# Kernel optimization log

Hardware: AMD Instinct MI355X
Metric: run time of the kernel (lower is better)

Reference implementation:

```python
import jax, jax.numpy as jnp
import numpy as np
import math

B, S, H, NH, WIN = 2, 2048, 1024, 16, 1024
HD = H // NH


def _ln(x, g, b, eps=1e-5):
    mu = jnp.mean(x, axis=-1, keepdims=True)
    var = jnp.var(x, axis=-1, keepdims=True)
    return (x - mu) * jax.lax.rsqrt(var + eps) * g + b


def setup_inputs() -> dict:
    key = jax.random.key(0)
    ks = jax.random.split(key, 16)
    w = lambda k, shp: jax.random.normal(k, shp, dtype=jnp.float32) * 0.02
    d = {
        "hidden_states": jax.random.normal(ks[0], (B, S, H), dtype=jnp.float32),
        "window_pos_bias": jax.random.normal(ks[1], (1, NH, 2 * WIN + 1, 2 * WIN + 1), dtype=jnp.float32) * 0.02,
        # position_encoding: Linear(1->H) + LayerNorm(H)
        "pe_w": w(ks[2], (1, H)), "pe_b": jnp.zeros((H,), jnp.float32),
        "pe_g": jnp.ones((H,), jnp.float32), "pe_beta": jnp.zeros((H,), jnp.float32),
        # pre-attention LayerNorm
        "norm_g": jnp.ones((H,), jnp.float32), "norm_b": jnp.zeros((H,), jnp.float32),
        # QKV projections (stored as [in, out])
        "Wq": w(ks[3], (H, H)), "bq": jnp.zeros((H,), jnp.float32),
        "Wk": w(ks[4], (H, H)), "bk": jnp.zeros((H,), jnp.float32),
        "Wv": w(ks[5], (H, H)), "bv": jnp.zeros((H,), jnp.float32),
        # out_proj: Linear(H,2H)+LN+ReLU, Linear(2H,2H)+LN+ReLU, Linear(2H,2H)+LN+ReLU, Linear(2H,H)
        "W1": w(ks[6], (H, 2 * H)), "b1": jnp.zeros((2 * H,), jnp.float32),
        "g1": jnp.ones((2 * H,), jnp.float32), "be1": jnp.zeros((2 * H,), jnp.float32),
        "W2": w(ks[7], (2 * H, 2 * H)), "b2": jnp.zeros((2 * H,), jnp.float32),
        "g2": jnp.ones((2 * H,), jnp.float32), "be2": jnp.zeros((2 * H,), jnp.float32),
        "W3": w(ks[8], (2 * H, 2 * H)), "b3": jnp.zeros((2 * H,), jnp.float32),
        "g3": jnp.ones((2 * H,), jnp.float32), "be3": jnp.zeros((2 * H,), jnp.float32),
        "W4": w(ks[9], (2 * H, H)), "b4": jnp.zeros((H,), jnp.float32),
    }
    return d


def reference(hidden_states, window_pos_bias, pe_w, pe_b, pe_g, pe_beta,
              norm_g, norm_b, Wq, bq, Wk, bk, Wv, bv,
              W1, b1, g1, be1, W2, b2, g2, be2, W3, b3, g3, be3, W4, b4):
    b, s, h = hidden_states.shape
    nh = window_pos_bias.shape[1]
    hd = h // nh
    # relative positions in [-1, 1): (i - s//2) / (s//2 + 1e-6)
    mid = s // 2
    pos = ((jnp.arange(s, dtype=jnp.float32) - mid) / (mid + 1e-6))[:, None]  # [s,1]
    pe = _ln(pos @ pe_w + pe_b, pe_g, pe_beta)  # [s,h]  (dropout = identity in eval)
    x = _ln(hidden_states + pe[None], norm_g, norm_b)
    q = (x @ Wq + bq).reshape(b, s, nh, hd)
    k = (x @ Wk + bk).reshape(b, s, nh, hd)
    v = (x @ Wv + bv).reshape(b, s, nh, hd)
    scores = jnp.einsum('bqhd,bkhd->bhqk', q, k) / math.sqrt(hd)
    if s <= window_pos_bias.shape[-1]:
        scores = scores + window_pos_bias[:, :, :s, :s]
    attn = jax.nn.softmax(scores, axis=-1)
    ctx = jnp.einsum('bhqk,bkhd->bqhd', attn, v).reshape(b, s, h)
    y = jax.nn.relu(_ln(ctx @ W1 + b1, g1, be1))
    y = jax.nn.relu(_ln(y @ W2 + b2, g2, be2))
    y = jax.nn.relu(_ln(y @ W3 + b3, g3, be3))
    out = y @ W4 + b4
    return out
```

## Files before the change

kernel.cpp:

```cpp
#include <hip/hip_runtime.h>
#include <hip/hip_bf16.h>
#include <stdint.h>
#include <math.h>

typedef unsigned short u16;
typedef unsigned int u32;
typedef __bf16 v8bf __attribute__((ext_vector_type(8)));
typedef float v4f __attribute__((ext_vector_type(4)));

constexpr int BATCH = 2;
constexpr int SEQ = 2048;
constexpr int HID = 1024;
constexpr int NHEAD = 16;
constexpr int HDIM = 64;
constexpr int MROWS = BATCH * SEQ;
constexpr int QKV_LD = 3 * HID;
constexpr int BIAS_LD = 2 * 1024 + 1;
constexpr size_t BIAS_HSTRIDE = (size_t)BIAS_LD * BIAS_LD;

__device__ __forceinline__ u16 f2bf(float f) {
    u32 u = __builtin_bit_cast(u32, f);
    u32 r = u + 0x7fffu + ((u >> 16) & 1u);
    return (u16)(r >> 16);
}
__device__ __forceinline__ float bf2f(u16 h) {
    return __builtin_bit_cast(float, (u32)h << 16);
}

__device__ __forceinline__ void gld16(const void* g, void* lds_base) {
    __builtin_amdgcn_global_load_lds(
        (const __attribute__((address_space(1))) u32*)(uintptr_t)g,
        (__attribute__((address_space(3))) u32*)(u32)(uintptr_t)lds_base,
        16, 0, 0);
}

__device__ __forceinline__ int swoff8(int row, int chunk)  { return (row * 8  + (chunk ^ (row & 7)))  << 4; }
__device__ __forceinline__ int swoff16(int row, int chunk) { return (row * 16 + (chunk ^ (row & 15))) << 4; }

__device__ __forceinline__ float2 blockreduce2(float a, float b) {
    #pragma unroll
    for (int m = 1; m < 64; m <<= 1) {
        a += __shfl_xor(a, m, 64);
        b += __shfl_xor(b, m, 64);
    }
    __shared__ float la[4], lb[4];
    int w = threadIdx.x >> 6;
    if ((threadIdx.x & 63) == 0) { la[w] = a; lb[w] = b; }
    __syncthreads();
    a = la[0] + la[1] + la[2] + la[3];
    b = lb[0] + lb[1] + lb[2] + lb[3];
    __syncthreads();
    return make_float2(a, b);
}

__global__ __launch_bounds__(256) void k_wt(const float* __restrict__ W, u16* __restrict__ Wt,
                                            int K, int N, float scale) {
    __shared__ float t[32][33];
    int n0 = blockIdx.x * 32, k0 = blockIdx.y * 32;
    int tx = threadIdx.x & 31, ty = threadIdx.x >> 5;
    #pragma unroll
    for (int i = 0; i < 32; i += 8) t[ty + i][tx] = W[(size_t)(k0 + ty + i) * N + n0 + tx];
    __syncthreads();
    #pragma unroll
    for (int i = 0; i < 32; i += 8) Wt[(size_t)(n0 + ty + i) * K + k0 + tx] = f2bf(t[tx][ty + i] * scale);
}

__global__ __launch_bounds__(256) void k_bcat(const float* __restrict__ bq, const float* __restrict__ bk,
                                              const float* __restrict__ bv, float* __restrict__ o) {
    int n = blockIdx.x * 256 + threadIdx.x;
    float v = (n < 1024) ? bq[n] * 0.125f : (n < 2048 ? bk[n - 1024] : bv[n - 2048]);
    o[n] = v;
}

__global__ __launch_bounds__(256) void k_prenorm(const float* __restrict__ hidden,
        const float* __restrict__ pe_w, const float* __restrict__ pe_b,
        const float* __restrict__ pe_g, const float* __restrict__ pe_beta,
        const float* __restrict__ ng, const float* __restrict__ nb, u16* __restrict__ xbf) {
    int row = blockIdx.x;
    int s = row & (SEQ - 1);
    float pos = ((float)s - 1024.0f) * (1.0f / 1024.0f);
    int t = threadIdx.x, hh = t * 4;
    float4 pw = *(const float4*)(pe_w + hh);
    float4 pb = *(const float4*)(pe_b + hh);
    float v[4] = { pos * pw.x + pb.x, pos * pw.y + pb.y, pos * pw.z + pb.z, pos * pw.w + pb.w };
    float s1 = 0.f, s2 = 0.f;
    #pragma unroll
    for (int i = 0; i < 4; i++) { s1 += v[i]; s2 += v[i] * v[i]; }
    float2 red = blockreduce2(s1, s2);
    float mean = red.x * (1.f / HID);
    float var  = red.y * (1.f / HID) - mean * mean;
    float rstd = rsqrtf(var + 1e-5f);
    float4 pg = *(const float4*)(pe_g + hh);
    float4 pbe = *(const float4*)(pe_beta + hh);
    float4 hv = *(const float4*)(hidden + (size_t)row * HID + hh);
    v[0] = hv.x + (v[0] - mean) * rstd * pg.x + pbe.x;
    v[1] = hv.y + (v[1] - mean) * rstd * pg.y + pbe.y;
    v[2] = hv.z + (v[2] - mean) * rstd * pg.z + pbe.z;
    v[3] = hv.w + (v[3] - mean) * rstd * pg.w + pbe.w;
    s1 = 0.f; s2 = 0.f;
    #pragma unroll
    for (int i = 0; i < 4; i++) { s1 += v[i]; s2 += v[i] * v[i]; }
    red = blockreduce2(s1, s2);
    mean = red.x * (1.f / HID);
    var  = red.y * (1.f / HID) - mean * mean;
    rstd = rsqrtf(var + 1e-5f);
    float4 gg = *(const float4*)(ng + hh);
    float4 bb = *(const float4*)(nb + hh);
    ushort4 o;
    o.x = f2bf((v[0] - mean) * rstd * gg.x + bb.x);
    o.y = f2bf((v[1] - mean) * rstd * gg.y + bb.y);
    o.z = f2bf((v[2] - mean) * rstd * gg.z + bb.z);
    o.w = f2bf((v[3] - mean) * rstd * gg.w + bb.w);
    *(ushort4*)(xbf + (size_t)row * HID + hh) = o;
}

__global__ __launch_bounds__(256) void k_ln_relu(const u16* __restrict__ Z,
        const float* __restrict__ g, const float* __restrict__ be, u16* __restrict__ Y) {
    const int N = 2048;
    int row = blockIdx.x, t = threadIdx.x, base = t * 8;
    union { uint4 q; u16 h[8]; } u;
    u.q = *(const uint4*)(Z + (size_t)row * N + base);
    float v[8];
    float s1 = 0.f, s2 = 0.f;
    #pragma unroll
    for (int i = 0; i < 8; i++) { v[i] = bf2f(u.h[i]); s1 += v[i]; s2 += v[i] * v[i]; }
    float2 red = blockreduce2(s1, s2);
    float mean = red.x * (1.f / N);
    float var  = red.y * (1.f / N) - mean * mean;
    float rstd = rsqrtf(var + 1e-5f);
    float4 g0 = *(const float4*)(g + base), g1 = *(const float4*)(g + base + 4);
    float4 b0 = *(const float4*)(be + base), b1 = *(const float4*)(be + base + 4);
    float gg[8] = { g0.x, g0.y, g0.z, g0.w, g1.x, g1.y, g1.z, g1.w };
    float bb[8] = { b0.x, b0.y, b0.z, b0.w, b1.x, b1.y, b1.z, b1.w };
    union { uint4 q; u16 h[8]; } o;
    #pragma unroll
    for (int i = 0; i < 8; i++) o.h[i] = f2bf(fmaxf((v[i] - mean) * rstd * gg[i] + bb[i], 0.f));
    *(uint4*)(Y + (size_t)row * N + base) = o.q;
}

__global__ __launch_bounds__(256) void k_vtrans(const u16* __restrict__ QKV, u16* __restrict__ Vt) {
    __shared__ u16 t[64][68];
    int s0 = blockIdx.x * 64, h = blockIdx.y, b = blockIdx.z;
    int x = threadIdx.x & 63, y = threadIdx.x >> 6;
    #pragma unroll
    for (int i = 0; i < 64; i += 4) {
        int r = i + y;
        t[r][x] = QKV[(size_t)(b * SEQ + s0 + r) * QKV_LD + 2048 + h * HDIM + x];
    }
    __syncthreads();
    size_t ob = (size_t)(b * NHEAD + h) * HDIM;
    #pragma unroll
    for (int i = 0; i < 64; i += 4) {
        int d = i + y;
        Vt[(ob + d) * SEQ + s0 + x] = t[x][d];
    }
}

template <int OUT_BF16>
__global__ __launch_bounds__(256, 3) void k_gemm(const u16* __restrict__ A, const u16* __restrict__ Bt,
        const float* __restrict__ bias, void* __restrict__ C, int N, int K) {
    __shared__ __align__(16) u16 lA[128 * 64];
    __shared__ __align__(16) u16 lB[128 * 64];
    char* lAc = (char*)lA;
    char* lBc = (char*)lB;
    const int m0 = blockIdx.x * 128, n0 = blockIdx.y * 128;
    const int tid = threadIdx.x, wave = tid >> 6, lane = tid & 63;
    const int wr = wave >> 1, wc = wave & 1, q4 = lane >> 4, ml = lane & 15;
    const int srow = wave * 8 + (lane >> 3);
    const int sqc  = (lane & 7) ^ (lane >> 3);

    v4f acc[4][4];
    v4f zz = {0.f, 0.f, 0.f, 0.f};
    #pragma unroll
    for (int i = 0; i < 4; i++)
        #pragma unroll
        for (int j = 0; j < 4; j++) acc[i][j] = zz;

    for (int k0 = 0; k0 < K; k0 += 64) {
        __syncthreads();
        #pragma unroll
        for (int it = 0; it < 4; it++) {
            int r = it * 32 + srow;
            gld16(A  + (size_t)(m0 + r) * K + k0 + sqc * 8, lAc + (it * 32 + wave * 8) * 128);
            gld16(Bt + (size_t)(n0 + r) * K + k0 + sqc * 8, lBc + (it * 32 + wave * 8) * 128);
        }
        __syncthreads();
        #pragma unroll
        for (int kk = 0; kk < 2; kk++) {
            v8bf af[4], bfv[4];
            #pragma unroll
            for (int i = 0; i < 4; i++) af[i] = *(const v8bf*)(lAc + swoff8(wr * 64 + i * 16 + ml, kk * 4 + q4));
            #pragma unroll
            for (int j = 0; j < 4; j++) bfv[j] = *(const v8bf*)(lBc + swoff8(wc * 64 + j * 16 + ml, kk * 4 + q4));
            #pragma unroll
            for (int i = 0; i < 4; i++)
                #pragma unroll
                for (int j = 0; j < 4; j++)
                    acc[i][j] = __builtin_amdgcn_mfma_f32_16x16x32_bf16(af[i], bfv[j], acc[i][j], 0, 0, 0);
        }
    }
    #pragma unroll
    for (int i = 0; i < 4; i++) {
        int rb = m0 + wr * 64 + i * 16 + q4 * 4;
        #pragma unroll
        for (int j = 0; j < 4; j++) {
            int col = n0 + wc * 64 + j * 16 + ml;
            float bv = bias[col];
            #pragma unroll
            for (int r = 0; r < 4; r++) {
                float val = acc[i][j][r] + bv;
                if (OUT_BF16) ((u16*)C)[(size_t)(rb + r) * N + col] = f2bf(val);
                else          ((float*)C)[(size_t)(rb + r) * N + col] = val;
            }
        }
    }
}

__global__ __launch_bounds__(256, 3) void k_attn(const u16* __restrict__ QKV,
        const u16* __restrict__ Vtm, const float* __restrict__ bias, u16* __restrict__ ctx) {
    __shared__ __align__(16) u16 lK[128 * 64];
    __shared__ __align__(16) u16 lP[4][16 * 128];
    int b = blockIdx.x, qt = blockIdx.y, h = blockIdx.z;
    int tid = threadIdx.x, wave = tid >> 6, lane = tid & 63;
    int q4 = lane >> 4, ml = lane & 15;
    char* lKc = (char*)lK;
    char* lPc = (char*)lP[wave];
    const int qbase = qt * 64 + wave * 16;
    const int srow = wave * 8 + (lane >> 3);
    const int sqc  = (lane & 7) ^ (lane >> 3);

    const u16* Qb = QKV + (size_t)(b * SEQ) * QKV_LD + h * HDIM;
    const u16* Kb = QKV + (size_t)(b * SEQ) * QKV_LD + 1024 + h * HDIM;
    const u16* Vb = Vtm + (size_t)(b * NHEAD + h) * HDIM * SEQ;
    const float* bh = bias + (size_t)h * BIAS_HSTRIDE;

    v8bf qf[2];
    #pragma unroll
    for (int kk = 0; kk < 2; kk++)
        qf[kk] = *(const v8bf*)(Qb + (size_t)(qbase + ml) * QKV_LD + kk * 32 + q4 * 8);

    float mr[4], lr[4];
    v4f o[4];
    v4f zz = {0.f, 0.f, 0.f, 0.f};
    #pragma unroll
    for (int r = 0; r < 4; r++) { mr[r] = -1e30f; lr[r] = 0.f; }
    #pragma unroll
    for (int n = 0; n < 4; n++) o[n] = zz;

    for (int kt = 0; kt < SEQ / 128; ++kt) {
        int k0 = kt * 128;
        __syncthreads();
        #pragma unroll
        for (int it = 0; it < 4; it++) {
            int r = it * 32 + srow;
            gld16(Kb + (size_t)(k0 + r) * QKV_LD + sqc * 8, lKc + (it * 32 + wave * 8) * 128);
        }
        float bv[4][8];
        const float* bp0 = bh + (size_t)(qbase + q4 * 4) * BIAS_LD + k0 + ml;
        #pragma unroll
        for (int r = 0; r < 4; r++)
            #pragma unroll
            for (int j = 0; j < 8; j++) bv[r][j] = bp0[(size_t)r * BIAS_LD + j * 16];
        __syncthreads();

        v4f sa[8];
        #pragma unroll
        for (int j = 0; j < 8; j++) sa[j] = zz;
        #pragma unroll
        for (int j = 0; j < 8; j++) {
            v8bf kf0 = *(const v8bf*)(lKc + swoff8(j * 16 + ml, q4));
            v8bf kf1 = *(const v8bf*)(lKc + swoff8(j * 16 + ml, 4 + q4));
            sa[j] = __builtin_amdgcn_mfma_f32_16x16x32_bf16(qf[0], kf0, sa[j], 0, 0, 0);
            sa[j] = __builtin_amdgcn_mfma_f32_16x16x32_bf16(qf[1], kf1, sa[j], 0, 0, 0);
        }
        #pragma unroll
        for (int r = 0; r < 4; r++) {
            float mx = -1e30f;
            #pragma unroll
            for (int j = 0; j < 8; j++) { sa[j][r] += bv[r][j]; mx = fmaxf(mx, sa[j][r]); }
            mx = fmaxf(mx, __shfl_xor(mx, 1, 64));
            mx = fmaxf(mx, __shfl_xor(mx, 2, 64));
            mx = fmaxf(mx, __shfl_xor(mx, 4, 64));
            mx = fmaxf(mx, __shfl_xor(mx, 8, 64));
            float mnew = fmaxf(mr[r], mx);
            float alpha = __expf(mr[r] - mnew);
            mr[r] = mnew;
            float rs = 0.f;
            #pragma unroll
            for (int j = 0; j < 8; j++) {
                float p = __expf(sa[j][r] - mnew);
                sa[j][r] = p;
                rs += p;
            }
            rs += __shfl_xor(rs, 1, 64);
            rs += __shfl_xor(rs, 2, 64);
            rs += __shfl_xor(rs, 4, 64);
            rs += __shfl_xor(rs, 8, 64);
            lr[r] = lr[r] * alpha + rs;
            #pragma unroll
            for (int n = 0; n < 4; n++) o[n][r] *= alpha;
        }
        #pragma unroll
        for (int j = 0; j < 8; j++) {
            int col = j * 16 + ml;
            #pragma unroll
            for (int r = 0; r < 4; r++) {
                int row = q4 * 4 + r;
                int off = row * 256 + (((col >> 3) ^ row) << 4) + ((col & 7) << 1);
                *(u16*)(lPc + off) = f2bf(sa[j][r]);
            }
        }
        v8bf vfc[4], vfn[4];
        #pragma unroll
        for (int n = 0; n < 4; n++)
            vfc[n] = *(const v8bf*)(Vb + (size_t)(n * 16 + ml) * SEQ + k0 + q4 * 8);
        #pragma unroll
        for (int kk = 0; kk < 4; kk++) {
            if (kk < 3) {
                #pragma unroll
                for (int n = 0; n < 4; n++)
                    vfn[n] = *(const v8bf*)(Vb + (size_t)(n * 16 + ml) * SEQ + k0 + (kk + 1) * 32 + q4 * 8);
            }
            v8bf pf = *(const v8bf*)(lPc + swoff16(ml, kk * 4 + q4));
            #pragma unroll
            for (int n = 0; n < 4; n++)
                o[n] = __builtin_amdgcn_mfma_f32_16x16x32_bf16(pf, vfc[n], o[n], 0, 0, 0);
            #pragma unroll
            for (int n = 0; n < 4; n++) vfc[n] = vfn[n];
        }
    }
    #pragma unroll
    for (int n = 0; n < 4; n++)
        #pragma unroll
        for (int r = 0; r < 4; r++) {
            size_t row = (size_t)(b * SEQ + qbase + q4 * 4 + r);
            ctx[row * HID + h * HDIM + n * 16 + ml] = f2bf(o[n][r] / lr[r]);
        }
}

extern "C" void kernel_launch(void* const* d_in, const int* in_sizes, int n_in,
                              void* d_out, int out_size, void* d_ws, size_t ws_size,
                              hipStream_t stream) {
    const float* hidden = (const float*)d_in[0];
    const float* wbias  = (const float*)d_in[1];
    const float* pe_w   = (const float*)d_in[2];
    const float* pe_b   = (const float*)d_in[3];
    const float* pe_g   = (const float*)d_in[4];
    const float* pe_be  = (const float*)d_in[5];
    const float* ng     = (const float*)d_in[6];
    const float* nb     = (const float*)d_in[7];
    const float* Wq = (const float*)d_in[8];  const float* bq = (const float*)d_in[9];
    const float* Wk = (const float*)d_in[10]; const float* bk = (const float*)d_in[11];
    const float* Wv = (const float*)d_in[12]; const float* bv = (const float*)d_in[13];
    const float* W1 = (const float*)d_in[14]; const float* b1 = (const float*)d_in[15];
    const float* g1 = (const float*)d_in[16]; const float* be1 = (const float*)d_in[17];
    const float* W2 = (const float*)d_in[18]; const float* b2 = (const float*)d_in[19];
    const float* g2 = (const float*)d_in[20]; const float* be2 = (const float*)d_in[21];
    const float* W3 = (const float*)d_in[22]; const float* b3 = (const float*)d_in[23];
    const float* g3 = (const float*)d_in[24]; const float* be3 = (const float*)d_in[25];
    const float* W4 = (const float*)d_in[26]; const float* b4 = (const float*)d_in[27];

    char* ws = (char*)d_ws;
    size_t off = 0;
    auto alloc = [&](size_t bytes) {
        char* p = ws + off;
        off += (bytes + 1023) & ~(size_t)1023;
        return p;
    };
    u16* wqkvt = (u16*)alloc((size_t)3072 * 1024 * 2);
    u16* w1t = (u16*)alloc((size_t)2048 * 1024 * 2);
    u16* w2t = (u16*)alloc((size_t)2048 * 2048 * 2);
    u16* w3t = (u16*)alloc((size_t)2048 * 2048 * 2);
    u16* w4t = (u16*)alloc((size_t)1024 * 2048 * 2);
    float* bqkv = (float*)alloc((size_t)3072 * 4);
    u16* xbf = (u16*)alloc((size_t)MROWS * HID * 2);
    u16* qkv = (u16*)alloc((size_t)MROWS * QKV_LD * 2);
    u16* vtb = (u16*)alloc((size_t)MROWS * HID * 2);
    u16* ctx = (u16*)alloc((size_t)MROWS * HID * 2);
    u16* zb  = (u16*)alloc((size_t)MROWS * 2048 * 2);
    u16* ya  = (u16*)alloc((size_t)MROWS * 2048 * 2);
    u16* yb  = (u16*)alloc((size_t)MROWS * 2048 * 2);

    dim3 blk(256);
    k_wt<<<dim3(32, 32), blk, 0, stream>>>(Wq, wqkvt, 1024, 1024, 0.125f);
    k_wt<<<dim3(32, 32), blk, 0, stream>>>(Wk, wqkvt + (size_t)1024 * 1024, 1024, 1024, 1.0f);
    k_wt<<<dim3(32, 32), blk, 0, stream>>>(Wv, wqkvt + (size_t)2048 * 1024, 1024, 1024, 1.0f);
    k_wt<<<dim3(64, 32), blk, 0, stream>>>(W1, w1t, 1024, 2048, 1.0f);
    k_wt<<<dim3(64, 64), blk, 0, stream>>>(W2, w2t, 2048, 2048, 1.0f);
    k_wt<<<dim3(64, 64), blk, 0, stream>>>(W3, w3t, 2048, 2048, 1.0f);
    k_wt<<<dim3(32, 64), blk, 0, stream>>>(W4, w4t, 2048, 1024, 1.0f);
    k_bcat<<<dim3(12), blk, 0, stream>>>(bq, bk, bv, bqkv);
    k_prenorm<<<MROWS, blk, 0, stream>>>(hidden, pe_w, pe_b, pe_g, pe_be, ng, nb, xbf);
    k_gemm<1><<<dim3(32, 24), blk, 0, stream>>>(xbf, wqkvt, bqkv, qkv, QKV_LD, 1024);
    k_vtrans<<<dim3(32, 16, 2), blk, 0, stream>>>(qkv, vtb);
    k_attn<<<dim3(2, 32, 16), blk, 0, stream>>>(qkv, vtb, wbias, ctx);
    k_gemm<1><<<dim3(32, 16), blk, 0, stream>>>(ctx, w1t, b1, zb, 2048, 1024);
    k_ln_relu<<<MROWS, blk, 0, stream>>>(zb, g1, be1, ya);
    k_gemm<1><<<dim3(32, 16), blk, 0, stream>>>(ya, w2t, b2, zb, 2048, 2048);
    k_ln_relu<<<MROWS, blk, 0, stream>>>(zb, g2, be2, yb);
    k_gemm<1><<<dim3(32, 16), blk, 0, stream>>>(yb, w3t, b3, zb, 2048, 2048);
    k_ln_relu<<<MROWS, blk, 0, stream>>>(zb, g3, be3, ya);
    k_gemm<0><<<dim3(32, 8), blk, 0, stream>>>(ya, w4t, b4, (float*)d_out, 1024, 2048);
}
```

Baseline: 897.9 us.

## Restructure attention kernel with transposed MFMA, direct K loads, vectorized bias

```diff
diff --git a/kernel.cpp b/kernel.cpp
--- a/kernel.cpp
+++ b/kernel.cpp
@@ -18,10 +18,15 @@
 constexpr int BIAS_LD = 2 * 1024 + 1;
 constexpr size_t BIAS_HSTRIDE = (size_t)BIAS_LD * BIAS_LD;
 
+struct f4u { float v[4]; };
+
 __device__ __forceinline__ u16 f2bf(float f) {
     u32 u = __builtin_bit_cast(u32, f);
     u32 r = u + 0x7fffu + ((u >> 16) & 1u);
     return (u16)(r >> 16);
+}
+__device__ __forceinline__ u16 f2bf_fast(float f) {
+    return (u16)((__builtin_bit_cast(u32, f) + 0x8000u) >> 16);
 }
 __device__ __forceinline__ float bf2f(u16 h) {
     return __builtin_bit_cast(float, (u32)h << 16);
@@ -35,7 +40,6 @@
 }
 
 __device__ __forceinline__ int swoff8(int row, int chunk)  { return (row * 8  + (chunk ^ (row & 7)))  << 4; }
-__device__ __forceinline__ int swoff16(int row, int chunk) { return (row * 16 + (chunk ^ (row & 15))) << 4; }
 
 __device__ __forceinline__ float2 blockreduce2(float a, float b) {
     #pragma unroll
@@ -216,126 +220,106 @@
     }
 }
 
-__global__ __launch_bounds__(256, 3) void k_attn(const u16* __restrict__ QKV,
+__global__ __launch_bounds__(256, 4) void k_attn(const u16* __restrict__ QKV,
         const u16* __restrict__ Vtm, const float* __restrict__ bias, u16* __restrict__ ctx) {
-    __shared__ __align__(16) u16 lK[128 * 64];
-    __shared__ __align__(16) u16 lP[4][16 * 128];
-    int b = blockIdx.x, qt = blockIdx.y, h = blockIdx.z;
-    int tid = threadIdx.x, wave = tid >> 6, lane = tid & 63;
-    int q4 = lane >> 4, ml = lane & 15;
-    char* lKc = (char*)lK;
+    __shared__ __align__(16) u16 lP[4][16 * 72];
+    const int b = blockIdx.x, qt = blockIdx.y, h = blockIdx.z;
+    const int tid = threadIdx.x, wave = tid >> 6, lane = tid & 63;
+    const int q4 = lane >> 4, ml = lane & 15;
     char* lPc = (char*)lP[wave];
     const int qbase = qt * 64 + wave * 16;
-    const int srow = wave * 8 + (lane >> 3);
-    const int sqc  = (lane & 7) ^ (lane >> 3);
 
     const u16* Qb = QKV + (size_t)(b * SEQ) * QKV_LD + h * HDIM;
     const u16* Kb = QKV + (size_t)(b * SEQ) * QKV_LD + 1024 + h * HDIM;
     const u16* Vb = Vtm + (size_t)(b * NHEAD + h) * HDIM * SEQ;
-    const float* bh = bias + (size_t)h * BIAS_HSTRIDE;
+    const float* brow = bias + (size_t)h * BIAS_HSTRIDE + (size_t)(qbase + ml) * BIAS_LD;
 
     v8bf qf[2];
     #pragma unroll
-    for (int kk = 0; kk < 2; kk++)
-        qf[kk] = *(const v8bf*)(Qb + (size_t)(qbase + ml) * QKV_LD + kk * 32 + q4 * 8);
-
-    float mr[4], lr[4];
+    for (int d0 = 0; d0 < 2; d0++)
+        qf[d0] = *(const v8bf*)(Qb + (size_t)(qbase + ml) * QKV_LD + d0 * 32 + q4 * 8);
+
+    float mr = -1e30f, lr = 0.f;
     v4f o[4];
     v4f zz = {0.f, 0.f, 0.f, 0.f};
     #pragma unroll
-    for (int r = 0; r < 4; r++) { mr[r] = -1e30f; lr[r] = 0.f; }
-    #pragma unroll
     for (int n = 0; n < 4; n++) o[n] = zz;
 
-    for (int kt = 0; kt < SEQ / 128; ++kt) {
-        int k0 = kt * 128;
-        __syncthreads();
-        #pragma unroll
-        for (int it = 0; it < 4; it++) {
-            int r = it * 32 + srow;
-            gld16(Kb + (size_t)(k0 + r) * QKV_LD + sqc * 8, lKc + (it * 32 + wave * 8) * 128);
-        }
-        float bv[4][8];
-        const float* bp0 = bh + (size_t)(qbase + q4 * 4) * BIAS_LD + k0 + ml;
-        #pragma unroll
-        for (int r = 0; r < 4; r++)
-            #pragma unroll
-            for (int j = 0; j < 8; j++) bv[r][j] = bp0[(size_t)r * BIAS_LD + j * 16];
-        __syncthreads();
-
-        v4f sa[8];
-        #pragma unroll
-        for (int j = 0; j < 8; j++) sa[j] = zz;
-        #pragma unroll
-        for (int j = 0; j < 8; j++) {
-            v8bf kf0 = *(const v8bf*)(lKc + swoff8(j * 16 + ml, q4));
-            v8bf kf1 = *(const v8bf*)(lKc + swoff8(j * 16 + ml, 4 + q4));
-            sa[j] = __builtin_amdgcn_mfma_f32_16x16x32_bf16(qf[0], kf0, sa[j], 0, 0, 0);
-            sa[j] = __builtin_amdgcn_mfma_f32_16x16x32_bf16(qf[1], kf1, sa[j], 0, 0, 0);
-        }
-        #pragma unroll
-        for (int r = 0; r < 4; r++) {
-            float mx = -1e30f;
-            #pragma unroll
-            for (int j = 0; j < 8; j++) { sa[j][r] += bv[r][j]; mx = fmaxf(mx, sa[j][r]); }
-            mx = fmaxf(mx, __shfl_xor(mx, 1, 64));
-            mx = fmaxf(mx, __shfl_xor(mx, 2, 64));
-            mx = fmaxf(mx, __shfl_xor(mx, 4, 64));
-            mx = fmaxf(mx, __shfl_xor(mx, 8, 64));
-            float mnew = fmaxf(mr[r], mx);
-            float alpha = __expf(mr[r] - mnew);
-            mr[r] = mnew;
-            float rs = 0.f;
-            #pragma unroll
-            for (int j = 0; j < 8; j++) {
+    f4u bv[4];
+    #pragma unroll
+    for (int j = 0; j < 4; j++) bv[j] = *(const f4u*)(brow + j * 16 + q4 * 4);
+
+    const int lpw = ml * 144;
+
+    for (int kt = 0; kt < SEQ / 64; ++kt) {
+        const int k0 = kt * 64;
+        v4f sa[4];
+        #pragma unroll
+        for (int jt = 0; jt < 4; jt++) {
+            v8bf kf0 = *(const v8bf*)(Kb + (size_t)(k0 + jt * 16 + ml) * QKV_LD + q4 * 8);
+            v8bf kf1 = *(const v8bf*)(Kb + (size_t)(k0 + jt * 16 + ml) * QKV_LD + 32 + q4 * 8);
+            sa[jt] = __builtin_amdgcn_mfma_f32_16x16x32_bf16(kf0, qf[0], zz, 0, 0, 0);
+            sa[jt] = __builtin_amdgcn_mfma_f32_16x16x32_bf16(kf1, qf[1], sa[jt], 0, 0, 0);
+        }
+        f4u bn[4];
+        if (kt < SEQ / 64 - 1) {
+            #pragma unroll
+            for (int j = 0; j < 4; j++) bn[j] = *(const f4u*)(brow + k0 + 64 + j * 16 + q4 * 4);
+        }
+        float mx = -1e30f;
+        #pragma unroll
+        for (int j = 0; j < 4; j++)
+            #pragma unroll
+            for (int r = 0; r < 4; r++) { sa[j][r] += bv[j].v[r]; mx = fmaxf(mx, sa[j][r]); }
+        mx = fmaxf(mx, __shfl_xor(mx, 16, 64));
+        mx = fmaxf(mx, __shfl_xor(mx, 32, 64));
+        float mnew = fmaxf(mr, mx);
+        float alpha = __expf(mr - mnew);
+        mr = mnew;
+        float rs = 0.f;
+        #pragma unroll
+        for (int j = 0; j < 4; j++)
+            #pragma unroll
+            for (int r = 0; r < 4; r++) {
                 float p = __expf(sa[j][r] - mnew);
                 sa[j][r] = p;
                 rs += p;
             }
-            rs += __shfl_xor(rs, 1, 64);
-            rs += __shfl_xor(rs, 2, 64);
-            rs += __shfl_xor(rs, 4, 64);
-            rs += __shfl_xor(rs, 8, 64);
-            lr[r] = lr[r] * alpha + rs;
-            #pragma unroll
-            for (int n = 0; n < 4; n++) o[n][r] *= alpha;
-        }
-        #pragma unroll
-        for (int j = 0; j < 8; j++) {
-            int col = j * 16 + ml;
-            #pragma unroll
-            for (int r = 0; r < 4; r++) {
-                int row = q4 * 4 + r;
-                int off = row * 256 + (((col >> 3) ^ row) << 4) + ((col & 7) << 1);
-                *(u16*)(lPc + off) = f2bf(sa[j][r]);
+        rs += __shfl_xor(rs, 16, 64);
+        rs += __shfl_xor(rs, 32, 64);
+        lr = lr * alpha + rs;
+        #pragma unroll
+        for (int n = 0; n < 4; n++) o[n] *= alpha;
+        #pragma unroll
+        for (int j = 0; j < 4; j++) {
+            uint2 pk;
+            pk.x = (u32)f2bf_fast(sa[j][0]) | ((u32)f2bf_fast(sa[j][1]) << 16);
+            pk.y = (u32)f2bf_fast(sa[j][2]) | ((u32)f2bf_fast(sa[j][3]) << 16);
+            *(uint2*)(lPc + lpw + j * 32 + q4 * 8) = pk;
+        }
+        #pragma unroll
+        for (int step = 0; step < 2; step++) {
+            v8bf pf = *(const v8bf*)(lPc + lpw + step * 64 + q4 * 16);
+            #pragma unroll
+            for (int n = 0; n < 4; n++) {
+                v8bf vf = *(const v8bf*)(Vb + (size_t)(n * 16 + ml) * SEQ + k0 + step * 32 + q4 * 8);
+                o[n] = __builtin_amdgcn_mfma_f32_16x16x32_bf16(vf, pf, o[n], 0, 0, 0);
             }
         }
-        v8bf vfc[4], vfn[4];
-        #pragma unroll
-        for (int n = 0; n < 4; n++)
-            vfc[n] = *(const v8bf*)(Vb + (size_t)(n * 16 + ml) * SEQ + k0 + q4 * 8);
-        #pragma unroll
-        for (int kk = 0; kk < 4; kk++) {
-            if (kk < 3) {
-                #pragma unroll
-                for (int n = 0; n < 4; n++)
-                    vfn[n] = *(const v8bf*)(Vb + (size_t)(n * 16 + ml) * SEQ + k0 + (kk + 1) * 32 + q4 * 8);
-            }
-            v8bf pf = *(const v8bf*)(lPc + swoff16(ml, kk * 4 + q4));
-            #pragma unroll
-            for (int n = 0; n < 4; n++)
-                o[n] = __builtin_amdgcn_mfma_f32_16x16x32_bf16(pf, vfc[n], o[n], 0, 0, 0);
-            #pragma unroll
-            for (int n = 0; n < 4; n++) vfc[n] = vfn[n];
-        }
-    }
-    #pragma unroll
-    for (int n = 0; n < 4; n++)
-        #pragma unroll
-        for (int r = 0; r < 4; r++) {
-            size_t row = (size_t)(b * SEQ + qbase + q4 * 4 + r);
-            ctx[row * HID + h * HDIM + n * 16 + ml] = f2bf(o[n][r] / lr[r]);
-        }
+        #pragma unroll
+        for (int j = 0; j < 4; j++) bv[j] = bn[j];
+    }
+    float inv = 1.0f / lr;
+    size_t rowb = (size_t)(b * SEQ + qbase + ml) * HID + h * HDIM + q4 * 4;
+    #pragma unroll
+    for (int n = 0; n < 4; n++) {
+        ushort4 st;
+        st.x = f2bf(o[n][0] * inv);
+        st.y = f2bf(o[n][1] * inv);
+        st.z = f2bf(o[n][2] * inv);
+        st.w = f2bf(o[n][3] * inv);
+        *(ushort4*)(ctx + rowb + n * 16) = st;
+    }
 }
 
 extern "C" void kernel_launch(void* const* d_in, const int* in_sizes, int n_in,
```

Measured after the change: 941.2 us. 4.8% more time.
